# Kernel optimization log

Hardware: AMD Instinct MI355X
Metric: run time of the kernel (lower is better)

Reference implementation:

```python
import jax, jax.numpy as jnp
import numpy as np


def setup_inputs() -> dict:
    key = jax.random.key(0)
    k1, k2 = jax.random.split(key)
    B, C, H, W = 4, 256, 64, 64
    f_m = jax.random.normal(k1, (B, C, H, W), dtype=jnp.float32)
    f_d = jax.random.normal(k2, (B, C, H, W), dtype=jnp.float32)
    return {"f_m": f_m, "f_d": f_d}


def reference(f_m, f_d):
    B, C, H, W = f_d.shape
    HW = H * W
    f_fuse = f_m + f_d                      # [B, C, H, W]
    f_c = f_fuse.reshape(B, C, HW)          # [B, C, HW]
    # scores[b, n, m] = sum_c f_c[b, c, n] * f_c[b, c, m]
    scores = jnp.einsum('bcn,bcm->bnm', f_c, f_c)   # [B, HW, HW]
    att = jax.nn.softmax(scores, axis=-1)           # softmax over last dim
    f_d_r = f_d.reshape(B, C, HW)                   # [B, C, HW]
    # out[b, c, m] = sum_n f_d_r[b, c, n] * att[b, n, m]
    f_d_att = jnp.einsum('bcn,bnm->bcm', f_d_r, att).reshape(B, C, H, W)
    return f_d_att + f_d
```

## Files before the change

kernel.cpp:

```cpp
#include <hip/hip_runtime.h>
#include <math.h>

#define B_ 4
#define C_ 256
#define N_ 4096
#define LDE 68
#define LDX 72

typedef __attribute__((ext_vector_type(8))) short short8;
typedef __attribute__((ext_vector_type(4))) float f32x4;
typedef __attribute__((ext_vector_type(2))) float f32x2;

__device__ inline ushort f2bf(float f) {
    uint u = __float_as_uint(f);
    return (ushort)((u + 0x7fffu + ((u >> 16) & 1u)) >> 16);
}
__device__ inline float bf2f(ushort h) { return __uint_as_float(((uint)h) << 16); }

__device__ inline f32x4 mfma16(short8 a, short8 b, f32x4 c) {
    return __builtin_amdgcn_mfma_f32_16x16x32_bf16(a, b, c, 0, 0, 0);
}
__device__ inline f32x4 mfma8(long a, long b, f32x4 c) {
    return __builtin_amdgcn_mfma_f32_16x16x32_fp8_fp8(a, b, c, 0, 0, 0);
}

__device__ inline size_t xfi8(int b, int nt, int kk) {
    return (((size_t)(b * 256 + nt)) * 8 + kk) * 512;
}
__device__ inline size_t ffi(int b, int nc, int ct, int k2) {
    return ((((size_t)(b * 64 + nc)) * 16 + ct) * 2 + k2) * 512;
}
__device__ inline size_t eti(int b, int mt, int ng) {
    return (((size_t)(b * 256 + mt)) * 512 + (size_t)ng) * 128;
}
__device__ inline size_t zmi(int b, int nc, int mt) {
    return ((size_t)(b * 64 + nc)) * 256 + mt;
}

__global__ __launch_bounds__(256) void prep_kernel(const float* __restrict__ fm,
                                                   const float* __restrict__ fd,
                                                   uchar* __restrict__ xfrag8,
                                                   ushort* __restrict__ ffrag) {
    __shared__ ushort xl[64][LDX];
    __shared__ ushort fl[64][LDX];
    const int b = blockIdx.z, c0 = blockIdx.y * 64, n0 = blockIdx.x * 64;
    const int t = threadIdx.x;
    const int n4 = (t & 15) * 4, cl = t >> 4;
    const size_t base = (size_t)b * C_ * N_;
    #pragma unroll
    for (int p = 0; p < 4; ++p) {
        const int cr = 16 * p + cl;
        const float4 m4 = *(const float4*)(fm + base + (size_t)(c0 + cr) * N_ + n0 + n4);
        const float4 d4 = *(const float4*)(fd + base + (size_t)(c0 + cr) * N_ + n0 + n4);
        ushort4 fo;
        fo.x = f2bf(d4.x); fo.y = f2bf(d4.y); fo.z = f2bf(d4.z); fo.w = f2bf(d4.w);
        *(ushort4*)(&fl[cr][n4]) = fo;
        ushort4 xo;
        xo.x = f2bf(m4.x + d4.x); xo.y = f2bf(m4.y + d4.y);
        xo.z = f2bf(m4.z + d4.z); xo.w = f2bf(m4.w + d4.w);
        *(ushort4*)(&xl[cr][n4]) = xo;
    }
    __syncthreads();
    const int l = t & 63, tl = t >> 6;
    {
        const int nl = 16 * tl + (l & 15);
        #pragma unroll
        for (int j = 0; j < 2; ++j) {
            const int kk = (c0 >> 5) + j;
            const int cb = 32 * j + 8 * (l >> 4);
            float f[8];
            #pragma unroll
            for (int i = 0; i < 8; ++i) f[i] = bf2f(xl[cb + i][nl]);
            int d0 = __builtin_amdgcn_cvt_pk_fp8_f32(f[0], f[1], 0, 0);
            d0 = __builtin_amdgcn_cvt_pk_fp8_f32(f[2], f[3], d0, 1);
            int d1 = __builtin_amdgcn_cvt_pk_fp8_f32(f[4], f[5], 0, 0);
            d1 = __builtin_amdgcn_cvt_pk_fp8_f32(f[6], f[7], d1, 1);
            uint* dst = (uint*)(xfrag8 + xfi8(b, (n0 >> 4) + tl, kk) + (size_t)l * 8);
            dst[0] = (uint)d0; dst[1] = (uint)d1;
        }
    }
    {
        const int row = 16 * tl + (l & 15);
        #pragma unroll
        for (int k2 = 0; k2 < 2; ++k2) {
            const int col = 32 * k2 + 8 * (l >> 4);
            const ushort4 a0 = *(const ushort4*)(&fl[row][col]);
            const ushort4 a1 = *(const ushort4*)(&fl[row][col + 4]);
            ushort* dst = ffrag + ffi(b, n0 >> 6, (c0 >> 4) + tl, k2) + l * 8;
            *(ushort4*)(dst) = a0; *(ushort4*)(dst + 4) = a1;
        }
    }
}

__global__ __launch_bounds__(512, 2) void lsum_e_kernel(const uchar* __restrict__ xfrag8,
                                                        ushort* __restrict__ ffrag,
                                                        uchar* __restrict__ E8,
                                                        uchar* __restrict__ zmask) {
    __shared__ float red[8][64];
    __shared__ float s_sh[64];
    const int bid = blockIdx.x;
    const int b = (bid >> 1) & 3;
    const int n0 = ((((bid >> 3) << 1) | (bid & 1))) * 64;
    const int t = threadIdx.x, lane = t & 63, w = t >> 6;
    const int l15 = lane & 15, q = lane >> 4;

    long af[4][8];
    #pragma unroll
    for (int ns = 0; ns < 4; ++ns)
        #pragma unroll
        for (int kk = 0; kk < 8; ++kk)
            af[ns][kk] = *(const long*)(xfrag8 + xfi8(b, (n0 >> 4) + ns, kk) + (size_t)lane * 8);

    float dv[4][4];
    #pragma unroll
    for (int ns = 0; ns < 4; ++ns) {
        f32x4 dacc = {0.f, 0.f, 0.f, 0.f};
        #pragma unroll
        for (int kk = 0; kk < 8; ++kk)
            dacc = mfma8(af[ns][kk], af[ns][kk], dacc);
        #pragma unroll
        for (int r = 0; r < 4; ++r)
            dv[ns][r] = __shfl(dacc[r], 20 * q + r, 64);
    }

    long bn[8];
    #pragma unroll
    for (int kk = 0; kk < 8; ++kk)
        bn[kk] = *(const long*)(xfrag8 + xfi8(b, w, kk) + (size_t)lane * 8);

    const size_t ebl = (size_t)l15 * 8 + 4 * (q & 1);
    const int ngb = (n0 >> 3) + (q >> 1);
    const int ncb = n0 >> 6;

    float rs[4][4] = {};
    for (int mc = 0; mc < 32; ++mc) {
        const int mtn = (mc + 1 < 32) ? (mc + 1) * 8 + w : w;
        f32x4 a0 = {0.f,0.f,0.f,0.f}, a1 = {0.f,0.f,0.f,0.f};
        f32x4 a2 = {0.f,0.f,0.f,0.f}, a3 = {0.f,0.f,0.f,0.f};
        #pragma unroll
        for (int kk = 0; kk < 8; ++kk) {
            const long bc = bn[kk];
            a0 = mfma8(af[0][kk], bc, a0);
            a1 = mfma8(af[1][kk], bc, a1);
            a2 = mfma8(af[2][kk], bc, a2);
            a3 = mfma8(af[3][kk], bc, a3);
            bn[kk] = *(const long*)(xfrag8 + xfi8(b, mtn, kk) + (size_t)lane * 8);
        }
        const int mt = mc * 8 + w;
        uint dpk[4];
#define EEXP(AA, NS)                                                                   \
        {                                                                              \
            float e0 = __expf(AA[0] - dv[NS][0]), e1 = __expf(AA[1] - dv[NS][1]);      \
            float e2 = __expf(AA[2] - dv[NS][2]), e3 = __expf(AA[3] - dv[NS][3]);      \
            rs[NS][0] += e0; rs[NS][1] += e1; rs[NS][2] += e2; rs[NS][3] += e3;        \
            int d = __builtin_amdgcn_cvt_pk_fp8_f32(e0, e1, 0, 0);                     \
            d = __builtin_amdgcn_cvt_pk_fp8_f32(e2, e3, d, 1);                         \
            dpk[NS] = (uint)d;                                                         \
        }
        EEXP(a0, 0) EEXP(a1, 1) EEXP(a2, 2) EEXP(a3, 3)
#undef EEXP
        const uint nzl = dpk[0] | dpk[1] | dpk[2] | dpk[3];
        const bool nz = (__ballot(nzl != 0u) != 0ULL);
        if (lane == 0) zmask[zmi(b, ncb, mt)] = nz ? 1 : 0;
        if (nz) {
            #pragma unroll
            for (int ns = 0; ns < 4; ++ns)
                *(uint*)(E8 + eti(b, mt, ngb + 2 * ns) + ebl) = dpk[ns];
        }
    }
    #pragma unroll
    for (int off = 1; off < 16; off <<= 1)
        #pragma unroll
        for (int ns = 0; ns < 4; ++ns)
            #pragma unroll
            for (int r = 0; r < 4; ++r)
                rs[ns][r] += __shfl_xor(rs[ns][r], off, 64);
    if (l15 == 0) {
        #pragma unroll
        for (int ns = 0; ns < 4; ++ns)
            #pragma unroll
            for (int r = 0; r < 4; ++r)
                red[w][16 * ns + 4 * q + r] = rs[ns][r];
    }
    __syncthreads();
    if (t < 64) {
        float s = 0.f;
        #pragma unroll
        for (int ww = 0; ww < 8; ++ww) s += red[ww][t];
        s_sh[t] = 1.0f / s;
    }
    __syncthreads();
    const int nc = n0 >> 6;
    #pragma unroll
    for (int ct2 = 0; ct2 < 2; ++ct2) {
        const int ct = 2 * w + ct2;
        #pragma unroll
        for (int k2 = 0; k2 < 2; ++k2) {
            ushort* fp = ffrag + ffi(b, nc, ct, k2) + (size_t)lane * 8;
            ushort4 u0 = *(ushort4*)fp;
            ushort4 u1 = *(ushort4*)(fp + 4);
            const int nb = 32 * k2 + 8 * q;
            ushort4 o0, o1;
            o0.x = f2bf(bf2f(u0.x) * s_sh[nb + 0]);
            o0.y = f2bf(bf2f(u0.y) * s_sh[nb + 1]);
            o0.z = f2bf(bf2f(u0.z) * s_sh[nb + 2]);
            o0.w = f2bf(bf2f(u0.w) * s_sh[nb + 3]);
            o1.x = f2bf(bf2f(u1.x) * s_sh[nb + 4]);
            o1.y = f2bf(bf2f(u1.y) * s_sh[nb + 5]);
            o1.z = f2bf(bf2f(u1.z) * s_sh[nb + 6]);
            o1.w = f2bf(bf2f(u1.w) * s_sh[nb + 7]);
            *(ushort4*)fp = o0;
            *(ushort4*)(fp + 4) = o1;
        }
    }
}

__global__ __launch_bounds__(512, 2) void out_e_kernel(const uchar* __restrict__ E8,
                                                       const ushort* __restrict__ ffrag,
                                                       const uchar* __restrict__ zmask,
                                                       const float* __restrict__ fd32,
                                                       float* __restrict__ outp) {
    const int bid = blockIdx.x;
    const int b = (bid >> 1) & 3;
    const int m0 = ((((bid >> 3) << 1) | (bid & 1))) * 64;
    const int t = threadIdx.x, lane = t & 63, w = t >> 6;
    const int l15 = lane & 15, q = lane >> 4;
    const size_t fb = (size_t)b * C_ * N_;
    const uchar* mrow = zmask + zmi(b, 0, m0 >> 4);

    f32x4 acc[2][4];
    #pragma unroll
    for (int ct = 0; ct < 2; ++ct)
        #pragma unroll
        for (int mt = 0; mt < 4; ++mt)
            acc[ct][mt] = (f32x4){0.f, 0.f, 0.f, 0.f};

    for (int g = 0; g < 8; ++g) {
        uint mk[8];
        #pragma unroll
        for (int i = 0; i < 8; ++i)
            mk[i] = *(const uint*)(mrow + (size_t)(8 * g + i) * 256);
        #pragma unroll
        for (int i = 0; i < 8; ++i) {
            if (mk[i] == 0) continue;
            const int nc = 8 * g + i;
            short8 fn[2][2];
            #pragma unroll
            for (int ct = 0; ct < 2; ++ct)
                #pragma unroll
                for (int k2 = 0; k2 < 2; ++k2)
                    fn[ct][k2] = *(const short8*)(ffrag + ffi(b, nc, 2 * w + ct, k2) + (size_t)lane * 8);
            #pragma unroll
            for (int k2 = 0; k2 < 2; ++k2) {
                #pragma unroll
                for (int mt = 0; mt < 4; ++mt) {
                    const long e8 = *(const long*)(E8 + eti(b, (m0 >> 4) + mt, 8 * nc + 4 * k2 + q) + (size_t)l15 * 8);
                    const uint lo = (uint)(unsigned long)e8;
                    const uint hi = (uint)((unsigned long)e8 >> 32);
                    const f32x2 f01 = __builtin_amdgcn_cvt_pk_f32_fp8((int)lo, false);
                    const f32x2 f23 = __builtin_amdgcn_cvt_pk_f32_fp8((int)lo, true);
                    const f32x2 f45 = __builtin_amdgcn_cvt_pk_f32_fp8((int)hi, false);
                    const f32x2 f67 = __builtin_amdgcn_cvt_pk_f32_fp8((int)hi, true);
                    union { uint u[4]; short8 v; } be;
                    asm("v_cvt_pk_bf16_f32 %0, %1, %2" : "=v"(be.u[0]) : "v"(f01.x), "v"(f01.y));
                    asm("v_cvt_pk_bf16_f32 %0, %1, %2" : "=v"(be.u[1]) : "v"(f23.x), "v"(f23.y));
                    asm("v_cvt_pk_bf16_f32 %0, %1, %2" : "=v"(be.u[2]) : "v"(f45.x), "v"(f45.y));
                    asm("v_cvt_pk_bf16_f32 %0, %1, %2" : "=v"(be.u[3]) : "v"(f67.x), "v"(f67.y));
                    acc[0][mt] = mfma16(fn[0][k2], be.v, acc[0][mt]);
                    acc[1][mt] = mfma16(fn[1][k2], be.v, acc[1][mt]);
                }
            }
        }
    }
    #pragma unroll
    for (int ct = 0; ct < 2; ++ct)
        #pragma unroll
        for (int mt = 0; mt < 4; ++mt)
            #pragma unroll
            for (int r = 0; r < 4; ++r) {
                const int c = 32 * w + 16 * ct + 4 * q + r;
                const int m = m0 + 16 * mt + l15;
                const size_t o = fb + (size_t)c * N_ + m;
                outp[o] = acc[ct][mt][r] + fd32[o];
            }
}

__global__ __launch_bounds__(512, 2) void lsum_g_kernel(const uchar* __restrict__ xfrag8,
                                                        float* __restrict__ lg) {
    __shared__ float red[8][64];
    __shared__ float dgl[64];
    const int bid = blockIdx.x;
    const int b = (bid >> 1) & 3;
    const int n0 = ((((bid >> 3) << 1) | (bid & 1))) * 64;
    const int t = threadIdx.x, lane = t & 63, w = t >> 6;
    const int l15 = lane & 15, q = lane >> 4;

    long af[4][8];
    #pragma unroll
    for (int ns = 0; ns < 4; ++ns)
        #pragma unroll
        for (int kk = 0; kk < 8; ++kk)
            af[ns][kk] = *(const long*)(xfrag8 + xfi8(b, (n0 >> 4) + ns, kk) + (size_t)lane * 8);

    float dv[4][4];
    #pragma unroll
    for (int ns = 0; ns < 4; ++ns) {
        f32x4 dacc = {0.f, 0.f, 0.f, 0.f};
        #pragma unroll
        for (int kk = 0; kk < 8; ++kk)
            dacc = mfma8(af[ns][kk], af[ns][kk], dacc);
        #pragma unroll
        for (int r = 0; r < 4; ++r)
            dv[ns][r] = __shfl(dacc[r], 20 * q + r, 64);
    }
    if (w == 0 && l15 == 0) {
        #pragma unroll
        for (int ns = 0; ns < 4; ++ns)
            #pragma unroll
            for (int r = 0; r < 4; ++r)
                dgl[16 * ns + 4 * q + r] = dv[ns][r];
    }

    long bn[8];
    #pragma unroll
    for (int kk = 0; kk < 8; ++kk)
        bn[kk] = *(const long*)(xfrag8 + xfi8(b, w, kk) + (size_t)lane * 8);

    float rs[4][4] = {};
    for (int mc = 0; mc < 32; ++mc) {
        const int mtn = (mc + 1 < 32) ? (mc + 1) * 8 + w : w;
        f32x4 a0 = {0.f,0.f,0.f,0.f}, a1 = {0.f,0.f,0.f,0.f};
        f32x4 a2 = {0.f,0.f,0.f,0.f}, a3 = {0.f,0.f,0.f,0.f};
        #pragma unroll
        for (int kk = 0; kk < 8; ++kk) {
            const long bc = bn[kk];
            a0 = mfma8(af[0][kk], bc, a0);
            a1 = mfma8(af[1][kk], bc, a1);
            a2 = mfma8(af[2][kk], bc, a2);
            a3 = mfma8(af[3][kk], bc, a3);
            bn[kk] = *(const long*)(xfrag8 + xfi8(b, mtn, kk) + (size_t)lane * 8);
        }
        #pragma unroll
        for (int r = 0; r < 4; ++r) {
            rs[0][r] += __expf(a0[r] - dv[0][r]);
            rs[1][r] += __expf(a1[r] - dv[1][r]);
            rs[2][r] += __expf(a2[r] - dv[2][r]);
            rs[3][r] += __expf(a3[r] - dv[3][r]);
        }
    }
    #pragma unroll
    for (int off = 1; off < 16; off <<= 1)
        #pragma unroll
        for (int ns = 0; ns < 4; ++ns)
            #pragma unroll
            for (int r = 0; r < 4; ++r)
                rs[ns][r] += __shfl_xor(rs[ns][r], off, 64);
    if (l15 == 0) {
        #pragma unroll
        for (int ns = 0; ns < 4; ++ns)
            #pragma unroll
            for (int r = 0; r < 4; ++r)
                red[w][16 * ns + 4 * q + r] = rs[ns][r];
    }
    __syncthreads();
    if (t < 64) {
        float s = 0.f;
        #pragma unroll
        for (int ww = 0; ww < 8; ++ww) s += red[ww][t];
        lg[b * N_ + n0 + t] = dgl[t] + __logf(s);
    }
}

__global__ __launch_bounds__(512, 2) void out_g_kernel(const uchar* __restrict__ xfrag8,
                                                       const ushort* __restrict__ ffrag,
                                                       const float* __restrict__ gg,
                                                       const float* __restrict__ fd32,
                                                       float* __restrict__ outp) {
    __shared__ ushort ET[2][64][LDE];
    const int bid = blockIdx.x;
    const int b = (bid >> 1) & 3;
    const int m0 = ((((bid >> 3) << 1) | (bid & 1))) * 64;
    const int t = threadIdx.x, lane = t & 63, w = t >> 6;
    const int l15 = lane & 15, q = lane >> 4;
    const int a = w & 3, h = w >> 2;
    const size_t fb = (size_t)b * C_ * N_;

    long bfr[2][8];
    #pragma unroll
    for (int jt = 0; jt < 2; ++jt)
        #pragma unroll
        for (int kk = 0; kk < 8; ++kk)
            bfr[jt][kk] = *(const long*)(xfrag8 + xfi8(b, (m0 >> 4) + 2 * h + jt, kk) + (size_t)lane * 8);

    f32x4 acc[2][4];
    #pragma unroll
    for (int ct = 0; ct < 2; ++ct)
        #pragma unroll
        for (int mt = 0; mt < 4; ++mt)
            acc[ct][mt] = (f32x4){0.f, 0.f, 0.f, 0.f};

    long an[8];
    #pragma unroll
    for (int kk = 0; kk < 8; ++kk)
        an[kk] = *(const long*)(xfrag8 + xfi8(b, a, kk) + (size_t)lane * 8);
    float gn[4];
    #pragma unroll
    for (int r = 0; r < 4; ++r) gn[r] = gg[b * N_ + 16 * a + 4 * q + r];

    int p = 0;
    for (int n0c = 0; n0c < N_; n0c += 64, p ^= 1) {
        const int nc = n0c >> 6;
        short8 fn[2][2];
        #pragma unroll
        for (int ct = 0; ct < 2; ++ct)
            #pragma unroll
            for (int k2 = 0; k2 < 2; ++k2)
                fn[ct][k2] = *(const short8*)(ffrag + ffi(b, nc, 2 * w + ct, k2) + lane * 8);
        float gv[4];
        #pragma unroll
        for (int r = 0; r < 4; ++r) gv[r] = gn[r];
        const int nx = (n0c + 64 < N_) ? n0c + 64 : 0;
        #pragma unroll
        for (int r = 0; r < 4; ++r) gn[r] = gg[b * N_ + nx + 16 * a + 4 * q + r];

        f32x4 s0 = {0.f, 0.f, 0.f, 0.f}, s1 = {0.f, 0.f, 0.f, 0.f};
        #pragma unroll
        for (int kk = 0; kk < 8; ++kk) {
            s0 = mfma8(an[kk], bfr[0][kk], s0);
            s1 = mfma8(an[kk], bfr[1][kk], s1);
            an[kk] = *(const long*)(xfrag8 + xfi8(b, (nx >> 4) + a, kk) + (size_t)lane * 8);
        }
        ushort4 e0, e1;
        e0.x = f2bf(__expf(s0[0] - gv[0])); e0.y = f2bf(__expf(s0[1] - gv[1]));
        e0.z = f2bf(__expf(s0[2] - gv[2])); e0.w = f2bf(__expf(s0[3] - gv[3]));
        e1.x = f2bf(__expf(s1[0] - gv[0])); e1.y = f2bf(__expf(s1[1] - gv[1]));
        e1.z = f2bf(__expf(s1[2] - gv[2])); e1.w = f2bf(__expf(s1[3] - gv[3]));
        *(ushort4*)(&ET[p][32 * h + l15][16 * a + 4 * q])      = e0;
        *(ushort4*)(&ET[p][32 * h + 16 + l15][16 * a + 4 * q]) = e1;

        asm volatile("s_waitcnt lgkmcnt(0)\n\ts_barrier" ::: "memory");

        #pragma unroll
        for (int k2 = 0; k2 < 2; ++k2) {
            #pragma unroll
            for (int mt = 0; mt < 4; ++mt) {
                const short8 be = *(const short8*)(&ET[p][16 * mt + l15][32 * k2 + 8 * q]);
                acc[0][mt] = mfma16(fn[0][k2], be, acc[0][mt]);
                acc[1][mt] = mfma16(fn[1][k2], be, acc[1][mt]);
            }
        }
    }
    #pragma unroll
    for (int ct = 0; ct < 2; ++ct)
        #pragma unroll
        for (int mt = 0; mt < 4; ++mt)
            #pragma unroll
            for (int r = 0; r < 4; ++r) {
                const int c = 32 * w + 16 * ct + 4 * q + r;
                const int m = m0 + 16 * mt + l15;
                const size_t o = fb + (size_t)c * N_ + m;
                outp[o] = acc[ct][mt][r] + fd32[o];
            }
}

extern "C" void kernel_launch(void* const* d_in, const int* in_sizes, int n_in,
                              void* d_out, int out_size, void* d_ws, size_t ws_size,
                              hipStream_t stream) {
    const float* fm = (const float*)d_in[0];
    const float* fd = (const float*)d_in[1];
    float* outp = (float*)d_out;

    const size_t xb_elts = (size_t)B_ * N_ * C_;
    const size_t e_bytes = (size_t)B_ * N_ * N_;
    const size_t z_bytes = (size_t)B_ * 64 * 256;
    const size_t need_e  = xb_elts * 3 + e_bytes + z_bytes;
    const size_t need_g  = xb_elts * 3 + (size_t)B_ * N_ * 4;

    uchar*  xfrag8 = (uchar*)d_ws;
    ushort* ffrag  = (ushort*)(xfrag8 + xb_elts);

    if (ws_size >= need_e) {
        uchar* E8 = (uchar*)(xfrag8 + xb_elts * 3);
        uchar* zmask = E8 + e_bytes;
        prep_kernel<<<dim3(N_ / 64, C_ / 64, B_), 256, 0, stream>>>(fm, fd, xfrag8, ffrag);
        lsum_e_kernel<<<dim3(256), 512, 0, stream>>>(xfrag8, ffrag, E8, zmask);
        out_e_kernel<<<dim3(256), 512, 0, stream>>>(E8, ffrag, zmask, fd, outp);
    } else if (ws_size >= need_g) {
        float* lg = (float*)(xfrag8 + xb_elts * 3);
        prep_kernel<<<dim3(N_ / 64, C_ / 64, B_), 256, 0, stream>>>(fm, fd, xfrag8, ffrag);
        lsum_g_kernel<<<dim3(256), 512, 0, stream>>>(xfrag8, lg);
        out_g_kernel<<<dim3(256), 512, 0, stream>>>(xfrag8, ffrag, lg, fd, outp);
    }
}
```

Measured before the change: 126.5 us.

## Drop bf16 f_d fragment buffer; scale f_d by inverse row sums in output kernel

```diff
diff --git a/kernel.cpp b/kernel.cpp
--- a/kernel.cpp
+++ b/kernel.cpp
@@ -37,12 +37,10 @@
     return ((size_t)(b * 64 + nc)) * 256 + mt;
 }
 
-__global__ __launch_bounds__(256) void prep_kernel(const float* __restrict__ fm,
-                                                   const float* __restrict__ fd,
-                                                   uchar* __restrict__ xfrag8,
-                                                   ushort* __restrict__ ffrag) {
+__global__ __launch_bounds__(256) void prep_x_kernel(const float* __restrict__ fm,
+                                                     const float* __restrict__ fd,
+                                                     uchar* __restrict__ xfrag8) {
     __shared__ ushort xl[64][LDX];
-    __shared__ ushort fl[64][LDX];
     const int b = blockIdx.z, c0 = blockIdx.y * 64, n0 = blockIdx.x * 64;
     const int t = threadIdx.x;
     const int n4 = (t & 15) * 4, cl = t >> 4;
@@ -52,9 +50,6 @@
         const int cr = 16 * p + cl;
         const float4 m4 = *(const float4*)(fm + base + (size_t)(c0 + cr) * N_ + n0 + n4);
         const float4 d4 = *(const float4*)(fd + base + (size_t)(c0 + cr) * N_ + n0 + n4);
-        ushort4 fo;
-        fo.x = f2bf(d4.x); fo.y = f2bf(d4.y); fo.z = f2bf(d4.z); fo.w = f2bf(d4.w);
-        *(ushort4*)(&fl[cr][n4]) = fo;
         ushort4 xo;
         xo.x = f2bf(m4.x + d4.x); xo.y = f2bf(m4.y + d4.y);
         xo.z = f2bf(m4.z + d4.z); xo.w = f2bf(m4.w + d4.w);
@@ -62,47 +57,34 @@
     }
     __syncthreads();
     const int l = t & 63, tl = t >> 6;
-    {
-        const int nl = 16 * tl + (l & 15);
-        #pragma unroll
-        for (int j = 0; j < 2; ++j) {
-            const int kk = (c0 >> 5) + j;
-            const int cb = 32 * j + 8 * (l >> 4);
-            float f[8];
-            #pragma unroll
-            for (int i = 0; i < 8; ++i) f[i] = bf2f(xl[cb + i][nl]);
-            int d0 = __builtin_amdgcn_cvt_pk_fp8_f32(f[0], f[1], 0, 0);
-            d0 = __builtin_amdgcn_cvt_pk_fp8_f32(f[2], f[3], d0, 1);
-            int d1 = __builtin_amdgcn_cvt_pk_fp8_f32(f[4], f[5], 0, 0);
-            d1 = __builtin_amdgcn_cvt_pk_fp8_f32(f[6], f[7], d1, 1);
-            uint* dst = (uint*)(xfrag8 + xfi8(b, (n0 >> 4) + tl, kk) + (size_t)l * 8);
-            dst[0] = (uint)d0; dst[1] = (uint)d1;
-        }
-    }
-    {
-        const int row = 16 * tl + (l & 15);
-        #pragma unroll
-        for (int k2 = 0; k2 < 2; ++k2) {
-            const int col = 32 * k2 + 8 * (l >> 4);
-            const ushort4 a0 = *(const ushort4*)(&fl[row][col]);
-            const ushort4 a1 = *(const ushort4*)(&fl[row][col + 4]);
-            ushort* dst = ffrag + ffi(b, n0 >> 6, (c0 >> 4) + tl, k2) + l * 8;
-            *(ushort4*)(dst) = a0; *(ushort4*)(dst + 4) = a1;
-        }
+    const int nl = 16 * tl + (l & 15);
+    #pragma unroll
+    for (int j = 0; j < 2; ++j) {
+        const int kk = (c0 >> 5) + j;
+        const int cb = 32 * j + 8 * (l >> 4);
+        float f[8];
+        #pragma unroll
+        for (int i = 0; i < 8; ++i) f[i] = bf2f(xl[cb + i][nl]);
+        int d0 = __builtin_amdgcn_cvt_pk_fp8_f32(f[0], f[1], 0, 0);
+        d0 = __builtin_amdgcn_cvt_pk_fp8_f32(f[2], f[3], d0, 1);
+        int d1 = __builtin_amdgcn_cvt_pk_fp8_f32(f[4], f[5], 0, 0);
+        d1 = __builtin_amdgcn_cvt_pk_fp8_f32(f[6], f[7], d1, 1);
+        uint* dst = (uint*)(xfrag8 + xfi8(b, (n0 >> 4) + tl, kk) + (size_t)l * 8);
+        dst[0] = (uint)d0; dst[1] = (uint)d1;
     }
 }
 
 __global__ __launch_bounds__(512, 2) void lsum_e_kernel(const uchar* __restrict__ xfrag8,
-                                                        ushort* __restrict__ ffrag,
                                                         uchar* __restrict__ E8,
-                                                        uchar* __restrict__ zmask) {
+                                                        uchar* __restrict__ zmask,
+                                                        float* __restrict__ sinv) {
     __shared__ float red[8][64];
-    __shared__ float s_sh[64];
     const int bid = blockIdx.x;
     const int b = (bid >> 1) & 3;
     const int n0 = ((((bid >> 3) << 1) | (bid & 1))) * 64;
     const int t = threadIdx.x, lane = t & 63, w = t >> 6;
     const int l15 = lane & 15, q = lane >> 4;
+    const int ph = (bid >> 3) & 31;
 
     long af[4][8];
     #pragma unroll
@@ -126,7 +108,7 @@
     long bn[8];
     #pragma unroll
     for (int kk = 0; kk < 8; ++kk)
-        bn[kk] = *(const long*)(xfrag8 + xfi8(b, w, kk) + (size_t)lane * 8);
+        bn[kk] = *(const long*)(xfrag8 + xfi8(b, (ph & 31) * 8 + w, kk) + (size_t)lane * 8);
 
     const size_t ebl = (size_t)l15 * 8 + 4 * (q & 1);
     const int ngb = (n0 >> 3) + (q >> 1);
@@ -134,7 +116,8 @@
 
     float rs[4][4] = {};
     for (int mc = 0; mc < 32; ++mc) {
-        const int mtn = (mc + 1 < 32) ? (mc + 1) * 8 + w : w;
+        const int cur = ((mc + ph) & 31) * 8 + w;
+        const int nxt = ((mc + 1 + ph) & 31) * 8 + w;
         f32x4 a0 = {0.f,0.f,0.f,0.f}, a1 = {0.f,0.f,0.f,0.f};
         f32x4 a2 = {0.f,0.f,0.f,0.f}, a3 = {0.f,0.f,0.f,0.f};
         #pragma unroll
@@ -144,9 +127,8 @@
             a1 = mfma8(af[1][kk], bc, a1);
             a2 = mfma8(af[2][kk], bc, a2);
             a3 = mfma8(af[3][kk], bc, a3);
-            bn[kk] = *(const long*)(xfrag8 + xfi8(b, mtn, kk) + (size_t)lane * 8);
-        }
-        const int mt = mc * 8 + w;
+            bn[kk] = *(const long*)(xfrag8 + xfi8(b, nxt, kk) + (size_t)lane * 8);
+        }
         uint dpk[4];
 #define EEXP(AA, NS)                                                                   \
         {                                                                              \
@@ -161,11 +143,11 @@
 #undef EEXP
         const uint nzl = dpk[0] | dpk[1] | dpk[2] | dpk[3];
         const bool nz = (__ballot(nzl != 0u) != 0ULL);
-        if (lane == 0) zmask[zmi(b, ncb, mt)] = nz ? 1 : 0;
+        if (lane == 0) zmask[zmi(b, ncb, cur)] = nz ? 1 : 0;
         if (nz) {
             #pragma unroll
             for (int ns = 0; ns < 4; ++ns)
-                *(uint*)(E8 + eti(b, mt, ngb + 2 * ns) + ebl) = dpk[ns];
+                *(uint*)(E8 + eti(b, cur, ngb + 2 * ns) + ebl) = dpk[ns];
         }
     }
     #pragma unroll
@@ -187,37 +169,13 @@
         float s = 0.f;
         #pragma unroll
         for (int ww = 0; ww < 8; ++ww) s += red[ww][t];
-        s_sh[t] = 1.0f / s;
-    }
-    __syncthreads();
-    const int nc = n0 >> 6;
-    #pragma unroll
-    for (int ct2 = 0; ct2 < 2; ++ct2) {
-        const int ct = 2 * w + ct2;
-        #pragma unroll
-        for (int k2 = 0; k2 < 2; ++k2) {
-            ushort* fp = ffrag + ffi(b, nc, ct, k2) + (size_t)lane * 8;
-            ushort4 u0 = *(ushort4*)fp;
-            ushort4 u1 = *(ushort4*)(fp + 4);
-            const int nb = 32 * k2 + 8 * q;
-            ushort4 o0, o1;
-            o0.x = f2bf(bf2f(u0.x) * s_sh[nb + 0]);
-            o0.y = f2bf(bf2f(u0.y) * s_sh[nb + 1]);
-            o0.z = f2bf(bf2f(u0.z) * s_sh[nb + 2]);
-            o0.w = f2bf(bf2f(u0.w) * s_sh[nb + 3]);
-            o1.x = f2bf(bf2f(u1.x) * s_sh[nb + 4]);
-            o1.y = f2bf(bf2f(u1.y) * s_sh[nb + 5]);
-            o1.z = f2bf(bf2f(u1.z) * s_sh[nb + 6]);
-            o1.w = f2bf(bf2f(u1.w) * s_sh[nb + 7]);
-            *(ushort4*)fp = o0;
-            *(ushort4*)(fp + 4) = o1;
-        }
+        sinv[b * N_ + n0 + t] = 1.0f / s;
     }
 }
 
 __global__ __launch_bounds__(512, 2) void out_e_kernel(const uchar* __restrict__ E8,
-                                                       const ushort* __restrict__ ffrag,
                                                        const uchar* __restrict__ zmask,
+                                                       const float* __restrict__ sinv,
                                                        const float* __restrict__ fd32,
                                                        float* __restrict__ outp) {
     const int bid = blockIdx.x;
@@ -244,12 +202,30 @@
         for (int i = 0; i < 8; ++i) {
             if (mk[i] == 0) continue;
             const int nc = 8 * g + i;
+            const float* sv = sinv + b * N_ + 64 * nc + 8 * q;
+            float4 s0[2], s1[2];
+            #pragma unroll
+            for (int k2 = 0; k2 < 2; ++k2) {
+                s0[k2] = *(const float4*)(sv + 32 * k2);
+                s1[k2] = *(const float4*)(sv + 32 * k2 + 4);
+            }
             short8 fn[2][2];
             #pragma unroll
-            for (int ct = 0; ct < 2; ++ct)
+            for (int ct = 0; ct < 2; ++ct) {
+                const int c = 32 * w + 16 * ct + l15;
+                const float* frow = fd32 + fb + (size_t)c * N_ + 64 * nc + 8 * q;
                 #pragma unroll
-                for (int k2 = 0; k2 < 2; ++k2)
-                    fn[ct][k2] = *(const short8*)(ffrag + ffi(b, nc, 2 * w + ct, k2) + (size_t)lane * 8);
+                for (int k2 = 0; k2 < 2; ++k2) {
+                    const float4 fa = *(const float4*)(frow + 32 * k2);
+                    const float4 fb4 = *(const float4*)(frow + 32 * k2 + 4);
+                    union { ushort us[8]; short8 v; } u;
+                    u.us[0] = f2bf(fa.x * s0[k2].x); u.us[1] = f2bf(fa.y * s0[k2].y);
+                    u.us[2] = f2bf(fa.z * s0[k2].z); u.us[3] = f2bf(fa.w * s0[k2].w);
+                    u.us[4] = f2bf(fb4.x * s1[k2].x); u.us[5] = f2bf(fb4.y * s1[k2].y);
+                    u.us[6] = f2bf(fb4.z * s1[k2].z); u.us[7] = f2bf(fb4.w * s1[k2].w);
+                    fn[ct][k2] = u.v;
+                }
+            }
             #pragma unroll
             for (int k2 = 0; k2 < 2; ++k2) {
                 #pragma unroll
@@ -285,6 +261,61 @@
             }
 }
 
+__global__ __launch_bounds__(256) void prep_kernel(const float* __restrict__ fm,
+                                                   const float* __restrict__ fd,
+                                                   uchar* __restrict__ xfrag8,
+                                                   ushort* __restrict__ ffrag) {
+    __shared__ ushort xl[64][LDX];
+    __shared__ ushort fl[64][LDX];
+    const int b = blockIdx.z, c0 = blockIdx.y * 64, n0 = blockIdx.x * 64;
+    const int t = threadIdx.x;
+    const int n4 = (t & 15) * 4, cl = t >> 4;
+    const size_t base = (size_t)b * C_ * N_;
+    #pragma unroll
+    for (int p = 0; p < 4; ++p) {
+        const int cr = 16 * p + cl;
+        const float4 m4 = *(const float4*)(fm + base + (size_t)(c0 + cr) * N_ + n0 + n4);
+        const float4 d4 = *(const float4*)(fd + base + (size_t)(c0 + cr) * N_ + n0 + n4);
+        ushort4 fo;
+        fo.x = f2bf(d4.x); fo.y = f2bf(d4.y); fo.z = f2bf(d4.z); fo.w = f2bf(d4.w);
+        *(ushort4*)(&fl[cr][n4]) = fo;
+        ushort4 xo;
+        xo.x = f2bf(m4.x + d4.x); xo.y = f2bf(m4.y + d4.y);
+        xo.z = f2bf(m4.z + d4.z); xo.w = f2bf(m4.w + d4.w);
+        *(ushort4*)(&xl[cr][n4]) = xo;
+    }
+    __syncthreads();
+    const int l = t & 63, tl = t >> 6;
+    {
+        const int nl = 16 * tl + (l & 15);
+        #pragma unroll
+        for (int j = 0; j < 2; ++j) {
+            const int kk = (c0 >> 5) + j;
+            const int cb = 32 * j + 8 * (l >> 4);
+            float f[8];
+            #pragma unroll
+            for (int i = 0; i < 8; ++i) f[i] = bf2f(xl[cb + i][nl]);
+            int d0 = __builtin_amdgcn_cvt_pk_fp8_f32(f[0], f[1], 0, 0);
+            d0 = __builtin_amdgcn_cvt_pk_fp8_f32(f[2], f[3], d0, 1);
+            int d1 = __builtin_amdgcn_cvt_pk_fp8_f32(f[4], f[5], 0, 0);
+            d1 = __builtin_amdgcn_cvt_pk_fp8_f32(f[6], f[7], d1, 1);
+            uint* dst = (uint*)(xfrag8 + xfi8(b, (n0 >> 4) + tl, kk) + (size_t)l * 8);
+            dst[0] = (uint)d0; dst[1] = (uint)d1;
+        }
+    }
+    {
+        const int row = 16 * tl + (l & 15);
+        #pragma unroll
+        for (int k2 = 0; k2 < 2; ++k2) {
+            const int col = 32 * k2 + 8 * (l >> 4);
+            const ushort4 a0 = *(const ushort4*)(&fl[row][col]);
+            const ushort4 a1 = *(const ushort4*)(&fl[row][col + 4]);
+            ushort* dst = ffrag + ffi(b, n0 >> 6, (c0 >> 4) + tl, k2) + l * 8;
+            *(ushort4*)(dst) = a0; *(ushort4*)(dst + 4) = a1;
+        }
+    }
+}
+
 __global__ __launch_bounds__(512, 2) void lsum_g_kernel(const uchar* __restrict__ xfrag8,
                                                         float* __restrict__ lg) {
     __shared__ float red[8][64];
@@ -473,20 +504,22 @@
     const size_t xb_elts = (size_t)B_ * N_ * C_;
     const size_t e_bytes = (size_t)B_ * N_ * N_;
     const size_t z_bytes = (size_t)B_ * 64 * 256;
-    const size_t need_e  = xb_elts * 3 + e_bytes + z_bytes;
+    const size_t s_bytes = (size_t)B_ * N_ * 4;
+    const size_t need_e  = xb_elts + e_bytes + z_bytes + s_bytes;
     const size_t need_g  = xb_elts * 3 + (size_t)B_ * N_ * 4;
 
-    uchar*  xfrag8 = (uchar*)d_ws;
-    ushort* ffrag  = (ushort*)(xfrag8 + xb_elts);
+    uchar* xfrag8 = (uchar*)d_ws;
 
     if (ws_size >= need_e) {
-        uchar* E8 = (uchar*)(xfrag8 + xb_elts * 3);
+        uchar* E8    = xfrag8 + xb_elts;
         uchar* zmask = E8 + e_bytes;
-        prep_kernel<<<dim3(N_ / 64, C_ / 64, B_), 256, 0, stream>>>(fm, fd, xfrag8, ffrag);
-        lsum_e_kernel<<<dim3(256), 512, 0, stream>>>(xfrag8, ffrag, E8, zmask);
-        out_e_kernel<<<dim3(256), 512, 0, stream>>>(E8, ffrag, zmask, fd, outp);
+        float* sinv  = (float*)(zmask + z_bytes);
+        prep_x_kernel<<<dim3(N_ / 64, C_ / 64, B_), 256, 0, stream>>>(fm, fd, xfrag8);
+        lsum_e_kernel<<<dim3(256), 512, 0, stream>>>(xfrag8, E8, zmask, sinv);
+        out_e_kernel<<<dim3(256), 512, 0, stream>>>(E8, zmask, sinv, fd, outp);
     } else if (ws_size >= need_g) {
-        float* lg = (float*)(xfrag8 + xb_elts * 3);
+        ushort* ffrag = (ushort*)(xfrag8 + xb_elts);
+        float*  lg    = (float*)(xfrag8 + xb_elts * 3);
         prep_kernel<<<dim3(N_ / 64, C_ / 64, B_), 256, 0, stream>>>(fm, fd, xfrag8, ffrag);
         lsum_g_kernel<<<dim3(256), 512, 0, stream>>>(xfrag8, lg);
         out_g_kernel<<<dim3(256), 512, 0, stream>>>(xfrag8, ffrag, lg, fd, outp);
```

After: 123.7 us. 1.02x faster.
